# Kernel optimization log

Hardware: AMD Instinct MI355X
Metric: run time of the kernel (lower is better)

## Reference

```python
import jax, jax.numpy as jnp
import numpy as np

EPS = 1e-06
CHUNK = 128  # chunkwise-recurrent block size for causal linear attention


def _feature_map(x):
    # elu(x) + 1, strictly positive kernel feature map
    return jax.nn.elu(x) + 1.0


def setup_inputs() -> dict:
    key = jax.random.key(0)
    kq, kk, kv = jax.random.split(key, 3)
    shape = (4, 4096, 16, 64)  # [N, L, H, D]
    return {
        "queries": jax.random.normal(kq, shape, dtype=jnp.float32),
        "keys": jax.random.normal(kk, shape, dtype=jnp.float32),
        "values": jax.random.normal(kv, shape, dtype=jnp.float32),
    }


def reference(queries, keys, values):
    # Causal linear attention: out_l = phi(q_l) . (sum_{s<=l} phi(k_s) v_s^T) / (phi(q_l) . sum_{s<=l} phi(k_s))
    q = _feature_map(queries)  # [N, L, H, D]
    k = _feature_map(keys)
    n, L, h, d = q.shape
    m = values.shape[-1]

    # Normalizer: z_l = q_l . cumsum(k)_l  (+ eps)
    z = jnp.einsum('nlhd,nlhd->nlh', q, jnp.cumsum(k, axis=1)) + EPS  # [N, L, H]

    # Chunkwise causal k (x) v accumulation
    g = L // CHUNK
    qc = q.reshape(n, g, CHUNK, h, d)
    kc = k.reshape(n, g, CHUNK, h, d)
    vc = values.reshape(n, g, CHUNK, h, m)

    # Per-chunk KV state and exclusive prefix over chunks
    kv = jnp.einsum('ngchd,ngchm->nghdm', kc, vc)  # [N, G, H, D, M]
    kv_cum = jnp.cumsum(kv, axis=1)
    kv_prev = jnp.concatenate([jnp.zeros_like(kv_cum[:, :1]), kv_cum[:, :-1]], axis=1)

    # Inter-chunk contribution (history before this chunk)
    inter = jnp.einsum('ngchd,nghdm->ngchm', qc, kv_prev)  # [N, G, C, H, M]

    # Intra-chunk causal contribution via lower-triangular masked scores
    scores = jnp.einsum('ngchd,ngkhd->nghck', qc, kc)  # [N, G, H, C, C]
    tri = jnp.tril(jnp.ones((CHUNK, CHUNK), dtype=bool))
    scores = jnp.where(tri[None, None, None], scores, 0.0)
    intra = jnp.einsum('nghck,ngkhm->ngchm', scores, vc)  # [N, G, C, H, M]

    num = (inter + intra).reshape(n, L, h, m)
    return num / z[..., None]
```

## Files before the change

kernel.cpp:

```cpp
#include <hip/hip_runtime.h>
#include <math.h>

static constexpr int Nn = 4, Ll = 4096, Hh = 16, Dd = 64, Mm = 64, Cc = 128, Gg = 32;
static constexpr int ROWS = Hh * Dd;
#define EPS_ 1e-6f

typedef __bf16 bf16x8 __attribute__((ext_vector_type(8)));
typedef unsigned short us8 __attribute__((ext_vector_type(8)));
typedef float f32x4 __attribute__((ext_vector_type(4)));

__device__ __forceinline__ float phi(float x) {
    return x > 0.0f ? x + 1.0f : __expf(x);
}

__device__ __forceinline__ unsigned short f2bf(float x) {
    unsigned u = __float_as_uint(x);
    return (unsigned short)((u + 0x7fffu + ((u >> 16) & 1u)) >> 16);
}
__device__ __forceinline__ float bf2f(unsigned short h) {
    return __uint_as_float(((unsigned)h) << 16);
}

#define MFMA16(A, B, C)                                                      \
    __builtin_amdgcn_mfma_f32_16x16x32_bf16(__builtin_bit_cast(bf16x8, (A)), \
                                            __builtin_bit_cast(bf16x8, (B)), \
                                            (C), 0, 0, 0)

__device__ __forceinline__ int KIDX(int j, int d) {
    return j * 64 + ((((d >> 3) ^ j) & 7) << 3) + (d & 7);
}
__device__ __forceinline__ int VTIDX(int m, int j) {
    return m * 128 + ((((j >> 3) ^ m) & 15) << 3) + (j & 7);
}
__device__ __forceinline__ int KVIDX(int m, int d) {
    return m * 64 + ((((d >> 3) ^ m) & 7) << 3) + (d & 7);
}
__device__ __forceinline__ int SIDX(int r, int j) {
    return r * 32 + ((((j >> 3) ^ (r >> 1)) & 3) << 3) + (j & 7);
}

__device__ __forceinline__ void load8(const float* p, float* xs) {
    float4 a = *(const float4*)p, b = *(const float4*)(p + 4);
    xs[0] = a.x; xs[1] = a.y; xs[2] = a.z; xs[3] = a.w;
    xs[4] = b.x; xs[5] = b.y; xs[6] = b.z; xs[7] = b.w;
}

__global__ __launch_bounds__(256) void kv_state_kernel(
    const float* __restrict__ keys, const float* __restrict__ values,
    float* __restrict__ kvbuf, float* __restrict__ ksumbuf)
{
    __shared__ alignas(16) unsigned short KthS[64 * 128];
    __shared__ alignas(16) unsigned short KtlS[64 * 128];
    __shared__ alignas(16) unsigned short VthS[64 * 128];
    __shared__ alignas(16) unsigned short VtlS[64 * 128];

    const int b = blockIdx.x;
    const int h = b % Hh;
    const int g = (b / Hh) % Gg;
    const int n = b / (Hh * Gg);
    const int tid = threadIdx.x;

    const size_t inbase = ((size_t)(n * Ll + g * Cc) * Hh + h) * Dd;

    for (int i = tid; i < 1024; i += 256) {
        const int jp = i >> 4, d4 = (i & 15) * 4;
        const int c0 = jp * 2;
        const float4 ka = *(const float4*)(keys   + inbase + (size_t)c0 * ROWS + d4);
        const float4 kb = *(const float4*)(keys   + inbase + (size_t)(c0 + 1) * ROWS + d4);
        const float4 va = *(const float4*)(values + inbase + (size_t)c0 * ROWS + d4);
        const float4 vb = *(const float4*)(values + inbase + (size_t)(c0 + 1) * ROWS + d4);
        const float kaa[4] = {ka.x, ka.y, ka.z, ka.w};
        const float kbb[4] = {kb.x, kb.y, kb.z, kb.w};
        const float vaa[4] = {va.x, va.y, va.z, va.w};
        const float vbb[4] = {vb.x, vb.y, vb.z, vb.w};
        #pragma unroll
        for (int e = 0; e < 4; ++e) {
            const int idx = VTIDX(d4 + e, c0);
            const float pa = phi(kaa[e]), pb = phi(kbb[e]);
            const unsigned ha = f2bf(pa), hb = f2bf(pb);
            *(unsigned*)(KthS + idx) = ha | (hb << 16);
            const unsigned la = f2bf(pa - bf2f((unsigned short)ha));
            const unsigned lb = f2bf(pb - bf2f((unsigned short)hb));
            *(unsigned*)(KtlS + idx) = la | (lb << 16);
            const unsigned hva = f2bf(vaa[e]), hvb = f2bf(vbb[e]);
            *(unsigned*)(VthS + idx) = hva | (hvb << 16);
            const unsigned lva = f2bf(vaa[e] - bf2f((unsigned short)hva));
            const unsigned lvb = f2bf(vbb[e] - bf2f((unsigned short)hvb));
            *(unsigned*)(VtlS + idx) = lva | (lvb << 16);
        }
    }
    __syncthreads();

    const int w = tid >> 6, l = tid & 63;
    const int lr = l & 15, lg = l >> 4;

    us8 ah[4], al[4];
    #pragma unroll
    for (int cs = 0; cs < 4; ++cs) {
        ah[cs] = *(const us8*)(VthS + VTIDX(w * 16 + lr, cs * 32 + lg * 8));
        al[cs] = *(const us8*)(VtlS + VTIDX(w * 16 + lr, cs * 32 + lg * 8));
    }

    float* kvout = kvbuf + ((size_t)((n * Gg + g) * Hh + h)) * (Dd * Mm);
    #pragma unroll
    for (int dt = 0; dt < 4; ++dt) {
        f32x4 acc = {0.f, 0.f, 0.f, 0.f};
        #pragma unroll
        for (int cs = 0; cs < 4; ++cs) {
            us8 bh = *(const us8*)(KthS + VTIDX(dt * 16 + lr, cs * 32 + lg * 8));
            us8 bl = *(const us8*)(KtlS + VTIDX(dt * 16 + lr, cs * 32 + lg * 8));
            acc = MFMA16(ah[cs], bh, acc);
            acc = MFMA16(ah[cs], bl, acc);
            acc = MFMA16(al[cs], bh, acc);
        }
        #pragma unroll
        for (int r = 0; r < 4; ++r)
            kvout[(size_t)(w * 16 + lg * 4 + r) * 64 + dt * 16 + lr] = acc[r];
    }

    if (tid < 64) {
        float s = 0.f;
        #pragma unroll
        for (int gb = 0; gb < 16; ++gb) {
            us8 hh = *(const us8*)(KthS + VTIDX(tid, gb * 8));
            us8 ll = *(const us8*)(KtlS + VTIDX(tid, gb * 8));
            #pragma unroll
            for (int e = 0; e < 8; ++e) s += bf2f(hh[e]) + bf2f(ll[e]);
        }
        ksumbuf[((size_t)((n * Gg + g) * Hh + h)) * 64 + tid] = s;
    }
}

__global__ __launch_bounds__(256) void prefix_kernel(
    float* __restrict__ kvbuf, float* __restrict__ ksumbuf)
{
    const int t = blockIdx.x * 256 + threadIdx.x;
    const int NKV = Nn * Hh * Dd * Mm;
    if (t < NKV) {
        const int nh = t >> 12, dm = t & 4095;
        const int n = nh >> 4, h = nh & 15;
        float run = 0.f;
        for (int g = 0; g < Gg; ++g) {
            const size_t idx = ((size_t)((n * Gg + g) * Hh + h)) * 4096 + dm;
            const float v = kvbuf[idx];
            kvbuf[idx] = run;
            run += v;
        }
    } else {
        const int t2 = t - NKV;
        if (t2 < Nn * Hh * Dd) {
            const int nh = t2 >> 6, d = t2 & 63;
            const int n = nh >> 4, h = nh & 15;
            float run = 0.f;
            for (int g = 0; g < Gg; ++g) {
                const size_t idx = ((size_t)((n * Gg + g) * Hh + h)) * 64 + d;
                const float v = ksumbuf[idx];
                ksumbuf[idx] = run;
                run += v;
            }
        }
    }
}

__global__ __launch_bounds__(256) void out_kernel(
    const float* __restrict__ queries,
    const float* __restrict__ keys,
    const float* __restrict__ values,
    const float* __restrict__ kvbuf,
    const float* __restrict__ ksumbuf,
    float* __restrict__ out)
{
    __shared__ alignas(16) unsigned short KhS[128 * 64];
    __shared__ alignas(16) unsigned short KlS[128 * 64];
    __shared__ alignas(16) unsigned short VthS[64 * 128];
    __shared__ alignas(16) unsigned short VtlS[64 * 128];
    __shared__ alignas(16) unsigned short KVhS[64 * 64];
    __shared__ alignas(16) unsigned short KVlS[64 * 64];
    __shared__ alignas(16) unsigned short SshS[4 * 2 * 512];
    __shared__ alignas(16) unsigned short SslS[4 * 2 * 512];
    __shared__ float kpreS[64];

    const int b = blockIdx.x;
    const int h = b & 15, g = (b >> 4) & 31, n = b >> 9;
    const int tid = threadIdx.x;

    const size_t chunkbase = ((size_t)(n * Ll + g * Cc) * Hh + h) * Dd;
    const size_t stateoff  = (size_t)((n * Gg + g) * Hh + h);

    if (tid < 16)
        *(float4*)(kpreS + tid * 4) =
            *(const float4*)(ksumbuf + stateoff * 64 + tid * 4);

    for (int t = tid; t < 1024; t += 256) {
        const int j = t >> 3, gb = t & 7;
        float xs[8];
        load8(keys + chunkbase + (size_t)j * ROWS + gb * 8, xs);
        us8 hh, ll;
        #pragma unroll
        for (int e = 0; e < 8; ++e) {
            const float p = phi(xs[e]);
            const unsigned short hb = f2bf(p);
            hh[e] = hb; ll[e] = f2bf(p - bf2f(hb));
        }
        const int base = KIDX(j, gb * 8);
        *(us8*)(KhS + base) = hh;
        *(us8*)(KlS + base) = ll;
    }
    for (int t = tid; t < 1024; t += 256) {
        const int jp = t >> 4, m4 = (t & 15) * 4;
        const int j0 = jp * 2;
        const float4 va = *(const float4*)(values + chunkbase + (size_t)j0 * ROWS + m4);
        const float4 vb = *(const float4*)(values + chunkbase + (size_t)(j0 + 1) * ROWS + m4);
        const float vaa[4] = {va.x, va.y, va.z, va.w};
        const float vbb[4] = {vb.x, vb.y, vb.z, vb.w};
        #pragma unroll
        for (int e = 0; e < 4; ++e) {
            const int idx = VTIDX(m4 + e, j0);
            const unsigned hva = f2bf(vaa[e]), hvb = f2bf(vbb[e]);
            *(unsigned*)(VthS + idx) = hva | (hvb << 16);
            const unsigned lva = f2bf(vaa[e] - bf2f((unsigned short)hva));
            const unsigned lvb = f2bf(vbb[e] - bf2f((unsigned short)hvb));
            *(unsigned*)(VtlS + idx) = lva | (lvb << 16);
        }
    }
    {
        const float* kvp = kvbuf + stateoff * (size_t)(Dd * Mm);
        for (int t = tid; t < 512; t += 256) {
            const int m = t >> 3, gb = t & 7;
            float xs[8];
            load8(kvp + m * 64 + gb * 8, xs);
            us8 hh, ll;
            #pragma unroll
            for (int e = 0; e < 8; ++e) {
                const unsigned short hb = f2bf(xs[e]);
                hh[e] = hb; ll[e] = f2bf(xs[e] - bf2f(hb));
            }
            const int base = KVIDX(m, gb * 8);
            *(us8*)(KVhS + base) = hh;
            *(us8*)(KVlS + base) = ll;
        }
    }
    __syncthreads();

    const int w = tid >> 6, l = tid & 63;
    const int lr = l & 15, lg = l >> 4;

    for (int tt = 0; tt < 2; ++tt) {
        const int T = tt ? (7 - w) : w;

        us8 qh[2], ql[2];
        float u = 0.f;
        #pragma unroll
        for (int ks = 0; ks < 2; ++ks) {
            float xs[8];
            load8(queries + chunkbase + (size_t)(T * 16 + lr) * ROWS + ks * 32 + lg * 8, xs);
            us8 hh, ll;
            #pragma unroll
            for (int e = 0; e < 8; ++e) {
                const float p = phi(xs[e]);
                u += p * kpreS[ks * 32 + lg * 8 + e];
                const unsigned short hb = f2bf(p);
                hh[e] = hb; ll[e] = f2bf(p - bf2f(hb));
            }
            qh[ks] = hh; ql[ks] = ll;
        }
        u += __shfl_xor(u, 16, 64);
        u += __shfl_xor(u, 32, 64);

        f32x4 accO[4];
        #pragma unroll
        for (int mt = 0; mt < 4; ++mt) {
            f32x4 acc = {0.f, 0.f, 0.f, 0.f};
            #pragma unroll
            for (int ks = 0; ks < 2; ++ks) {
                us8 bh = *(const us8*)(KVhS + KVIDX(mt * 16 + lr, ks * 32 + lg * 8));
                us8 bl = *(const us8*)(KVlS + KVIDX(mt * 16 + lr, ks * 32 + lg * 8));
                acc = MFMA16(qh[ks], bh, acc);
                acc = MFMA16(qh[ks], bl, acc);
                acc = MFMA16(ql[ks], bh, acc);
            }
            accO[mt] = acc;
        }

        f32x4 zp = {0.f, 0.f, 0.f, 0.f};
        const int nJb = (T + 2) >> 1;
        for (int Jb = 0; Jb < nJb; ++Jb) {
            const int Jlo = 2 * Jb, Jhi = 2 * Jb + 1;
            const bool hasHi = (Jhi <= T);

            f32x4 slo = {0.f, 0.f, 0.f, 0.f};
            f32x4 shi = {0.f, 0.f, 0.f, 0.f};
            #pragma unroll
            for (int ks = 0; ks < 2; ++ks) {
                us8 bh = *(const us8*)(KhS + KIDX(Jlo * 16 + lr, ks * 32 + lg * 8));
                us8 bl = *(const us8*)(KlS + KIDX(Jlo * 16 + lr, ks * 32 + lg * 8));
                slo = MFMA16(qh[ks], bh, slo);
                slo = MFMA16(qh[ks], bl, slo);
                slo = MFMA16(ql[ks], bh, slo);
            }
            if (hasHi) {
                #pragma unroll
                for (int ks = 0; ks < 2; ++ks) {
                    us8 bh = *(const us8*)(KhS + KIDX(Jhi * 16 + lr, ks * 32 + lg * 8));
                    us8 bl = *(const us8*)(KlS + KIDX(Jhi * 16 + lr, ks * 32 + lg * 8));
                    shi = MFMA16(qh[ks], bh, shi);
                    shi = MFMA16(qh[ks], bl, shi);
                    shi = MFMA16(ql[ks], bh, shi);
                }
            }
            if (Jlo == T) {
                #pragma unroll
                for (int r = 0; r < 4; ++r)
                    if (lr > lg * 4 + r) slo[r] = 0.f;
            }
            if (hasHi && Jhi == T) {
                #pragma unroll
                for (int r = 0; r < 4; ++r)
                    if (lr > lg * 4 + r) shi[r] = 0.f;
            }
            zp += slo;
            zp += shi;

            unsigned short* sh = SshS + (w * 2 + (Jb & 1)) * 512;
            unsigned short* sl = SslS + (w * 2 + (Jb & 1)) * 512;
            #pragma unroll
            for (int r = 0; r < 4; ++r) {
                const int row = lg * 4 + r;
                const unsigned short h0 = f2bf(slo[r]);
                sh[SIDX(row, lr)] = h0;
                sl[SIDX(row, lr)] = f2bf(slo[r] - bf2f(h0));
                const unsigned short h1 = f2bf(shi[r]);
                sh[SIDX(row, 16 + lr)] = h1;
                sl[SIDX(row, 16 + lr)] = f2bf(shi[r] - bf2f(h1));
            }
            asm volatile("s_waitcnt lgkmcnt(0)" ::: "memory");
            __builtin_amdgcn_sched_barrier(0);

            us8 ah = *(const us8*)(sh + SIDX(lr, lg * 8));
            us8 al = *(const us8*)(sl + SIDX(lr, lg * 8));
            #pragma unroll
            for (int mt = 0; mt < 4; ++mt) {
                us8 vh = *(const us8*)(VthS + VTIDX(mt * 16 + lr, Jb * 32 + lg * 8));
                us8 vl = *(const us8*)(VtlS + VTIDX(mt * 16 + lr, Jb * 32 + lg * 8));
                accO[mt] = MFMA16(ah, vh, accO[mt]);
                accO[mt] = MFMA16(ah, vl, accO[mt]);
                accO[mt] = MFMA16(al, vh, accO[mt]);
            }
        }

        #pragma unroll
        for (int r = 0; r < 4; ++r) {
            float s = zp[r];
            s += __shfl_xor(s, 1, 64);
            s += __shfl_xor(s, 2, 64);
            s += __shfl_xor(s, 4, 64);
            s += __shfl_xor(s, 8, 64);
            zp[r] = s;
        }

        const size_t ob = ((size_t)(n * Ll + g * Cc + T * 16) * Hh + h) * Mm;
        #pragma unroll
        for (int r = 0; r < 4; ++r) {
            const int row = lg * 4 + r;
            const float ur = __shfl(u, row, 64);
            const float iz = 1.0f / (EPS_ + ur + zp[r]);
            #pragma unroll
            for (int mt = 0; mt < 4; ++mt)
                out[ob + (size_t)row * ROWS + mt * 16 + lr] = accO[mt][r] * iz;
        }
    }
}

extern "C" void kernel_launch(void* const* d_in, const int* in_sizes, int n_in,
                              void* d_out, int out_size, void* d_ws, size_t ws_size,
                              hipStream_t stream) {
    const float* q = (const float*)d_in[0];
    const float* k = (const float*)d_in[1];
    const float* v = (const float*)d_in[2];
    float* out = (float*)d_out;

    float* kvbuf   = (float*)d_ws;
    float* ksumbuf = kvbuf + (size_t)Nn * Gg * Hh * Dd * Mm;

    kv_state_kernel<<<Nn * Gg * Hh, 256, 0, stream>>>(k, v, kvbuf, ksumbuf);

    const int nseries = Nn * Hh * Dd * Mm + Nn * Hh * Dd;
    prefix_kernel<<<nseries / 256, 256, 0, stream>>>(kvbuf, ksumbuf);

    out_kernel<<<Nn * Gg * Hh, 256, 0, stream>>>(q, k, v, kvbuf, ksumbuf, out);
}
```

Baseline: 316.2 us.

## Pre-split KV prefix into packed bf16 hi/lo and read directly in out kernel

The prefix kernel now writes the exclusive KV prefix as packed bf16 hi/lo pairs, and out_kernel reads them straight from global memory with perm-based unpacking. This removes the LDS staging of the KV state and its fp32-to-bf16 split. The change also removes the double-buffering and swizzle of the score scratch, adds s_setprio around the MFMA blocks, sets launch_bounds occupancy to 2, and alters the VTIDX swizzle. It risks extra global-load latency inside the per-tile loop. Without the Jb parity buffer, a single per-wave score buffer could also be overwritten while other lanes are still reading it.

```diff
diff --git a/kernel.cpp b/kernel.cpp
--- a/kernel.cpp
+++ b/kernel.cpp
@@ -30,13 +30,7 @@
     return j * 64 + ((((d >> 3) ^ j) & 7) << 3) + (d & 7);
 }
 __device__ __forceinline__ int VTIDX(int m, int j) {
-    return m * 128 + ((((j >> 3) ^ m) & 15) << 3) + (j & 7);
-}
-__device__ __forceinline__ int KVIDX(int m, int d) {
-    return m * 64 + ((((d >> 3) ^ m) & 7) << 3) + (d & 7);
-}
-__device__ __forceinline__ int SIDX(int r, int j) {
-    return r * 32 + ((((j >> 3) ^ (r >> 1)) & 3) << 3) + (j & 7);
+    return m * 128 + ((((j >> 3) ^ (m & 15) ^ (m >> 4)) & 15) << 3) + (j & 7);
 }
 
 __device__ __forceinline__ void load8(const float* p, float* xs) {
@@ -45,7 +39,22 @@
     xs[4] = b.x; xs[5] = b.y; xs[6] = b.z; xs[7] = b.w;
 }
 
-__global__ __launch_bounds__(256) void kv_state_kernel(
+__device__ __forceinline__ void unpack8(const unsigned* p, us8& hi, us8& lo) {
+    const uint4 a = *(const uint4*)p;
+    const uint4 b = *(const uint4*)(p + 4);
+    union { unsigned u[4]; us8 v; } H, L;
+    H.u[0] = __builtin_amdgcn_perm(a.y, a.x, 0x05040100u);
+    L.u[0] = __builtin_amdgcn_perm(a.y, a.x, 0x07060302u);
+    H.u[1] = __builtin_amdgcn_perm(a.w, a.z, 0x05040100u);
+    L.u[1] = __builtin_amdgcn_perm(a.w, a.z, 0x07060302u);
+    H.u[2] = __builtin_amdgcn_perm(b.y, b.x, 0x05040100u);
+    L.u[2] = __builtin_amdgcn_perm(b.y, b.x, 0x07060302u);
+    H.u[3] = __builtin_amdgcn_perm(b.w, b.z, 0x05040100u);
+    L.u[3] = __builtin_amdgcn_perm(b.w, b.z, 0x07060302u);
+    hi = H.v; lo = L.v;
+}
+
+__global__ __launch_bounds__(256, 2) void kv_state_kernel(
     const float* __restrict__ keys, const float* __restrict__ values,
     float* __restrict__ kvbuf, float* __restrict__ ksumbuf)
 {
@@ -102,6 +111,7 @@
     }
 
     float* kvout = kvbuf + ((size_t)((n * Gg + g) * Hh + h)) * (Dd * Mm);
+    __builtin_amdgcn_s_setprio(1);
     #pragma unroll
     for (int dt = 0; dt < 4; ++dt) {
         f32x4 acc = {0.f, 0.f, 0.f, 0.f};
@@ -117,6 +127,7 @@
         for (int r = 0; r < 4; ++r)
             kvout[(size_t)(w * 16 + lg * 4 + r) * 64 + dt * 16 + lr] = acc[r];
     }
+    __builtin_amdgcn_s_setprio(0);
 
     if (tid < 64) {
         float s = 0.f;
@@ -139,11 +150,14 @@
     if (t < NKV) {
         const int nh = t >> 12, dm = t & 4095;
         const int n = nh >> 4, h = nh & 15;
+        unsigned* kvp = (unsigned*)kvbuf;
         float run = 0.f;
         for (int g = 0; g < Gg; ++g) {
             const size_t idx = ((size_t)((n * Gg + g) * Hh + h)) * 4096 + dm;
             const float v = kvbuf[idx];
-            kvbuf[idx] = run;
+            const unsigned hb = f2bf(run);
+            const unsigned lb = f2bf(run - bf2f((unsigned short)hb));
+            kvp[idx] = hb | (lb << 16);
             run += v;
         }
     } else {
@@ -162,7 +176,7 @@
     }
 }
 
-__global__ __launch_bounds__(256) void out_kernel(
+__global__ __launch_bounds__(256, 2) void out_kernel(
     const float* __restrict__ queries,
     const float* __restrict__ keys,
     const float* __restrict__ values,
@@ -174,10 +188,8 @@
     __shared__ alignas(16) unsigned short KlS[128 * 64];
     __shared__ alignas(16) unsigned short VthS[64 * 128];
     __shared__ alignas(16) unsigned short VtlS[64 * 128];
-    __shared__ alignas(16) unsigned short KVhS[64 * 64];
-    __shared__ alignas(16) unsigned short KVlS[64 * 64];
-    __shared__ alignas(16) unsigned short SshS[4 * 2 * 512];
-    __shared__ alignas(16) unsigned short SslS[4 * 2 * 512];
+    __shared__ alignas(16) unsigned short SshS[4 * 512];
+    __shared__ alignas(16) unsigned short SslS[4 * 512];
     __shared__ float kpreS[64];
 
     const int b = blockIdx.x;
@@ -223,27 +235,11 @@
             *(unsigned*)(VtlS + idx) = lva | (lvb << 16);
         }
     }
-    {
-        const float* kvp = kvbuf + stateoff * (size_t)(Dd * Mm);
-        for (int t = tid; t < 512; t += 256) {
-            const int m = t >> 3, gb = t & 7;
-            float xs[8];
-            load8(kvp + m * 64 + gb * 8, xs);
-            us8 hh, ll;
-            #pragma unroll
-            for (int e = 0; e < 8; ++e) {
-                const unsigned short hb = f2bf(xs[e]);
-                hh[e] = hb; ll[e] = f2bf(xs[e] - bf2f(hb));
-            }
-            const int base = KVIDX(m, gb * 8);
-            *(us8*)(KVhS + base) = hh;
-            *(us8*)(KVlS + base) = ll;
-        }
-    }
     __syncthreads();
 
     const int w = tid >> 6, l = tid & 63;
     const int lr = l & 15, lg = l >> 4;
+    const unsigned* kvpk = (const unsigned*)kvbuf + stateoff * (size_t)4096;
 
     for (int tt = 0; tt < 2; ++tt) {
         const int T = tt ? (7 - w) : w;
@@ -270,15 +266,17 @@
         f32x4 accO[4];
         #pragma unroll
         for (int mt = 0; mt < 4; ++mt) {
+            const unsigned* p = kvpk + (size_t)(mt * 16 + lr) * 64 + lg * 8;
+            us8 bh0, bl0, bh1, bl1;
+            unpack8(p, bh0, bl0);
+            unpack8(p + 32, bh1, bl1);
             f32x4 acc = {0.f, 0.f, 0.f, 0.f};
-            #pragma unroll
-            for (int ks = 0; ks < 2; ++ks) {
-                us8 bh = *(const us8*)(KVhS + KVIDX(mt * 16 + lr, ks * 32 + lg * 8));
-                us8 bl = *(const us8*)(KVlS + KVIDX(mt * 16 + lr, ks * 32 + lg * 8));
-                acc = MFMA16(qh[ks], bh, acc);
-                acc = MFMA16(qh[ks], bl, acc);
-                acc = MFMA16(ql[ks], bh, acc);
-            }
+            acc = MFMA16(qh[0], bh0, acc);
+            acc = MFMA16(qh[0], bl0, acc);
+            acc = MFMA16(ql[0], bh0, acc);
+            acc = MFMA16(qh[1], bh1, acc);
+            acc = MFMA16(qh[1], bl1, acc);
+            acc = MFMA16(ql[1], bh1, acc);
             accO[mt] = acc;
         }
 
@@ -290,6 +288,7 @@
 
             f32x4 slo = {0.f, 0.f, 0.f, 0.f};
             f32x4 shi = {0.f, 0.f, 0.f, 0.f};
+            __builtin_amdgcn_s_setprio(1);
             #pragma unroll
             for (int ks = 0; ks < 2; ++ks) {
                 us8 bh = *(const us8*)(KhS + KIDX(Jlo * 16 + lr, ks * 32 + lg * 8));
@@ -308,6 +307,7 @@
                     shi = MFMA16(ql[ks], bh, shi);
                 }
             }
+            __builtin_amdgcn_s_setprio(0);
             if (Jlo == T) {
                 #pragma unroll
                 for (int r = 0; r < 4; ++r)
@@ -321,23 +321,24 @@
             zp += slo;
             zp += shi;
 
-            unsigned short* sh = SshS + (w * 2 + (Jb & 1)) * 512;
-            unsigned short* sl = SslS + (w * 2 + (Jb & 1)) * 512;
+            unsigned short* sh = SshS + w * 512;
+            unsigned short* sl = SslS + w * 512;
             #pragma unroll
             for (int r = 0; r < 4; ++r) {
                 const int row = lg * 4 + r;
                 const unsigned short h0 = f2bf(slo[r]);
-                sh[SIDX(row, lr)] = h0;
-                sl[SIDX(row, lr)] = f2bf(slo[r] - bf2f(h0));
+                sh[row * 32 + lr]      = h0;
+                sl[row * 32 + lr]      = f2bf(slo[r] - bf2f(h0));
                 const unsigned short h1 = f2bf(shi[r]);
-                sh[SIDX(row, 16 + lr)] = h1;
-                sl[SIDX(row, 16 + lr)] = f2bf(shi[r] - bf2f(h1));
+                sh[row * 32 + 16 + lr] = h1;
+                sl[row * 32 + 16 + lr] = f2bf(shi[r] - bf2f(h1));
             }
             asm volatile("s_waitcnt lgkmcnt(0)" ::: "memory");
             __builtin_amdgcn_sched_barrier(0);
 
-            us8 ah = *(const us8*)(sh + SIDX(lr, lg * 8));
-            us8 al = *(const us8*)(sl + SIDX(lr, lg * 8));
+            us8 ah = *(const us8*)(sh + lr * 32 + lg * 8);
+            us8 al = *(const us8*)(sl + lr * 32 + lg * 8);
+            __builtin_amdgcn_s_setprio(1);
             #pragma unroll
             for (int mt = 0; mt < 4; ++mt) {
                 us8 vh = *(const us8*)(VthS + VTIDX(mt * 16 + lr, Jb * 32 + lg * 8));
@@ -346,6 +347,7 @@
                 accO[mt] = MFMA16(ah, vl, accO[mt]);
                 accO[mt] = MFMA16(al, vh, accO[mt]);
             }
+            __builtin_amdgcn_s_setprio(0);
         }
 
         #pragma unroll
```

Result: faster. 285.8 us (-9.6%).
